# Optimization experiments

Hardware: AMD Instinct MI355X
Metric: run time of the kernel (lower is better)

## Reference

```python
import jax, jax.numpy as jnp
import numpy as np

DIM = 64
SQRT_DIM = float(np.sqrt(DIM))


def setup_inputs() -> dict:
    rng = jax.random.key(0)
    k1, k2, k3, k4 = jax.random.split(rng, 4)
    B, S, D = 16, 2048, DIM
    query = jax.random.normal(k1, (B, S, D), dtype=jnp.float32)
    key = jax.random.normal(k2, (B, S, D), dtype=jnp.float32)
    value = jax.random.normal(k3, (B, S, D), dtype=jnp.float32)
    mask = jax.random.randint(k4, (B, S), 0, 2) == 1  # True = masked (pad)
    return {"query": query, "key": key, "value": value, "mask": mask}


def reference(query, key, value, mask):
    # score: [B, S, S]
    score = jnp.einsum('bsd,btd->bst', query, key) / SQRT_DIM
    # symmetric mask: position (i, j) masked if token i OR token j is padded
    m = jnp.logical_or(mask[:, :, None], mask[:, None, :])  # [B, S, S]
    score = jnp.where(m, -jnp.inf, score)
    attn = jax.nn.softmax(score, axis=-1)
    attn = jnp.where(m, 0.0, attn)
    context = jnp.einsum('bst,btd->bsd', attn, value)
    return (context, attn)
```

## Files before the change

### kernel.cpp

```cpp
#include <hip/hip_runtime.h>
#include <hip/hip_bf16.h>

#define NBATCH 16
#define SLEN   2048
#define DIM    64
#define TQ     64
#define NTHR   256
#define NW     4
#define PANEL  128
#define NPANEL (SLEN / PANEL)
#define PROWP  136
#define PROWK  72
#define PROWV  136

typedef __attribute__((ext_vector_type(8))) short bf16x8;
typedef __attribute__((ext_vector_type(4))) float f32x4;

__device__ inline short f2bf(float f) {
    union { __hip_bfloat16 h; short s; } u;
    u.h = __float2bfloat16(f);
    return u.s;
}
__device__ inline float bf2f(unsigned short s) {
    union { unsigned u; float f; } x;
    x.u = ((unsigned)s) << 16;
    return x.f;
}
__device__ inline bf16x8 pack8(float4 a, float4 b) {
    bf16x8 r;
    r[0] = f2bf(a.x); r[1] = f2bf(a.y); r[2] = f2bf(a.z); r[3] = f2bf(a.w);
    r[4] = f2bf(b.x); r[5] = f2bf(b.y); r[6] = f2bf(b.z); r[7] = f2bf(b.w);
    return r;
}
__device__ inline bf16x8 pack8s(float4 a, float4 b, float s) {
    bf16x8 r;
    r[0] = f2bf(a.x * s); r[1] = f2bf(a.y * s); r[2] = f2bf(a.z * s); r[3] = f2bf(a.w * s);
    r[4] = f2bf(b.x * s); r[5] = f2bf(b.y * s); r[6] = f2bf(b.z * s); r[7] = f2bf(b.w * s);
    return r;
}

__global__ __launch_bounds__(256) void preconvert_kernel(
    const float* __restrict__ K, const float* __restrict__ V,
    short* __restrict__ Kws, short* __restrict__ VTws)
{
    const int b  = blockIdx.x >> 4;
    const int p  = blockIdx.x & 15;
    const int j0 = p * PANEL;
    const int tid = threadIdx.x;
    const float* Kb = K + ((size_t)b * SLEN + j0) * DIM;
    const float* Vb = V + ((size_t)b * SLEN + j0) * DIM;
    short* Kwb  = Kws  + ((size_t)b * SLEN + j0) * DIM;
    short* VTwb = VTws + (size_t)b * DIM * SLEN;

    #pragma unroll
    for (int it = 0; it < 8; it++) {
        const int idx = it * 256 + tid;
        const int row = idx >> 4, c4 = idx & 15;
        float4 kv = *(const float4*)(Kb + (size_t)row * DIM + c4 * 4);
        const int blk = (c4 >> 1) ^ (row & 7);
        *(short4*)(Kwb + (size_t)row * DIM + blk * 8 + (c4 & 1) * 4) =
            make_short4(f2bf(kv.x), f2bf(kv.y), f2bf(kv.z), f2bf(kv.w));
    }
    #pragma unroll
    for (int it = 0; it < 2; it++) {
        const int task = it * 256 + tid;
        const int k4 = task >> 4, d4 = (task & 15) * 4;
        const int kb = k4 * 4;
        const float* vp = Vb + (size_t)kb * DIM + d4;
        float4 r0 = *(const float4*)(vp);
        float4 r1 = *(const float4*)(vp + DIM);
        float4 r2 = *(const float4*)(vp + 2 * DIM);
        float4 r3 = *(const float4*)(vp + 3 * DIM);
        const int qn = kb >> 3, hw = kb & 7;
        *(short4*)(VTwb + (size_t)(d4 + 0) * SLEN + j0 + ((qn ^ ((d4 + 0) & 7)) * 8) + hw) =
            make_short4(f2bf(r0.x), f2bf(r1.x), f2bf(r2.x), f2bf(r3.x));
        *(short4*)(VTwb + (size_t)(d4 + 1) * SLEN + j0 + ((qn ^ ((d4 + 1) & 7)) * 8) + hw) =
            make_short4(f2bf(r0.y), f2bf(r1.y), f2bf(r2.y), f2bf(r3.y));
        *(short4*)(VTwb + (size_t)(d4 + 2) * SLEN + j0 + ((qn ^ ((d4 + 2) & 7)) * 8) + hw) =
            make_short4(f2bf(r0.z), f2bf(r1.z), f2bf(r2.z), f2bf(r3.z));
        *(short4*)(VTwb + (size_t)(d4 + 3) * SLEN + j0 + ((qn ^ ((d4 + 3) & 7)) * 8) + hw) =
            make_short4(f2bf(r0.w), f2bf(r1.w), f2bf(r2.w), f2bf(r3.w));
    }
}

__device__ __forceinline__ void stage_k_panel(const short* __restrict__ Kwb, int j0,
                                              short* sdst, int w, int l) {
    const short* src = Kwb + (size_t)j0 * DIM + w * 512 + l * 8;
    short* dst = sdst + w * 512;
    #pragma unroll
    for (int i = 0; i < 4; i++)
        __builtin_amdgcn_global_load_lds((const unsigned int*)(src + i * 2048),
                                         (unsigned int*)(dst + i * 2048), 16, 0, 0);
}
__device__ __forceinline__ void stage_v_panel(const short* __restrict__ VTwb, int j0,
                                              short* sdst, int w, int l) {
    #pragma unroll
    for (int i = 0; i < 4; i++) {
        const int d0 = (w * 4 + i) * 4;
        __builtin_amdgcn_global_load_lds(
            (const unsigned int*)(VTwb + (size_t)(d0 + (l >> 4)) * SLEN + j0 + (l & 15) * 8),
            (unsigned int*)(sdst + d0 * PANEL), 16, 0, 0);
    }
}

#define MFMA16(a, bb, cc) __builtin_amdgcn_mfma_f32_16x16x32_bf16((a), (bb), (cc), 0, 0, 0)

__global__ __launch_bounds__(NTHR, 3) void sdpa_kernel(
    const float* __restrict__ Q, const short* __restrict__ Kws,
    const short* __restrict__ VTws, const int* __restrict__ M,
    float* __restrict__ outCtx, float* __restrict__ outAttn)
{
    __shared__ __align__(16) short sK[PANEL * DIM];
    __shared__ __align__(16) short sVT[DIM * PANEL];
    __shared__ __align__(16) short sP[NW * 16 * PROWP];
    __shared__ short sMaskBf[SLEN];

    const int tid = threadIdx.x;
    const int w = tid >> 6, l = tid & 63, g = l >> 4, c = l & 15;
    const int wg = (blockIdx.x & 7) * (NBATCH * (SLEN / TQ) / 8) + (blockIdx.x >> 3);
    const int b  = wg >> 5;
    const int i0 = (wg & 31) * TQ;
    const int i0w = i0 + w * 16;

    const short* Kwb  = Kws  + (size_t)b * SLEN * DIM;
    const short* VTwb = VTws + (size_t)b * DIM * SLEN;
    const int*   Mb   = M + b * SLEN;

    bf16x8 qa0, qa1;
    {
        const float* qp = Q + ((size_t)b * SLEN + i0w + c) * DIM + g * 8;
        qa0 = pack8s(*(const float4*)(qp),      *(const float4*)(qp + 4),  0.125f);
        qa1 = pack8s(*(const float4*)(qp + 32), *(const float4*)(qp + 36), 0.125f);
    }

    stage_k_panel(Kwb, 0, sK, w, l);
    #pragma unroll
    for (int i = 0; i < 8; i++) {
        const int idx = i * NTHR + tid;
        sMaskBf[idx] = Mb[idx] ? (short)0 : (short)0x3F80;
    }
    __syncthreads();

    float rsum[4] = {0.f, 0.f, 0.f, 0.f};
    for (int p = 0; p < NPANEL; p++) {
        const short* cur = (p & 1) ? sVT : sK;
        if (p < NPANEL - 1)
            stage_k_panel(Kwb, (p + 1) * PANEL, (p & 1) ? sK : sVT, w, l);
        const int j0 = p * PANEL;
        #pragma unroll
        for (int jt = 0; jt < 8; jt++) {
            const short* kr = cur + (jt * 16 + c) * DIM;
            bf16x8 kb0 = *(const bf16x8*)(kr + ((g ^ (c & 7)) * 8));
            bf16x8 kb1 = *(const bf16x8*)(kr + (((g + 4) ^ (c & 7)) * 8));
            f32x4 acc = {0.f, 0.f, 0.f, 0.f};
            acc = MFMA16(qa0, kb0, acc);
            acc = MFMA16(qa1, kb1, acc);
            const float em = bf2f((unsigned short)sMaskBf[j0 + jt * 16 + c]);
            #pragma unroll
            for (int r = 0; r < 4; r++)
                rsum[r] += __expf(acc[r]) * em;
        }
        __syncthreads();
    }

    stage_k_panel(Kwb, 0, sK, w, l);
    stage_v_panel(VTwb, 0, sVT, w, l);

    #pragma unroll
    for (int off = 1; off < 16; off <<= 1) {
        #pragma unroll
        for (int r = 0; r < 4; r++)
            rsum[r] += __shfl_xor(rsum[r], off, 64);
    }
    float scv[4];
    #pragma unroll
    for (int r = 0; r < 4; r++) {
        const bool rm = sMaskBf[i0w + g * 4 + r] == 0;
        scv[r] = (rm || rsum[r] <= 0.f) ? 0.f : 1.f / rsum[r];
    }

    short* sPw = sP + w * 16 * PROWP;
    f32x4 pv[4];
    #pragma unroll
    for (int nt = 0; nt < 4; nt++) pv[nt] = (f32x4){0.f, 0.f, 0.f, 0.f};

    __syncthreads();

    for (int p = 0; p < NPANEL; p++) {
        const int j0 = p * PANEL;
        #pragma unroll
        for (int jt = 0; jt < 8; jt++) {
            const short* kr = sK + (jt * 16 + c) * DIM;
            bf16x8 kb0 = *(const bf16x8*)(kr + ((g ^ (c & 7)) * 8));
            bf16x8 kb1 = *(const bf16x8*)(kr + (((g + 4) ^ (c & 7)) * 8));
            f32x4 acc = {0.f, 0.f, 0.f, 0.f};
            acc = MFMA16(qa0, kb0, acc);
            acc = MFMA16(qa1, kb1, acc);
            const float em = bf2f((unsigned short)sMaskBf[j0 + jt * 16 + c]);
            #pragma unroll
            for (int r = 0; r < 4; r++)
                sPw[(g * 4 + r) * PROWP + jt * 16 + c] =
                    f2bf(__expf(acc[r]) * em * scv[r]);
        }
        #pragma unroll
        for (int ks = 0; ks < 4; ks++) {
            bf16x8 af = *(const bf16x8*)(sPw + c * PROWP + ks * 32 + g * 8);
            #pragma unroll
            for (int nt = 0; nt < 4; nt++) {
                const int d = nt * 16 + c;
                bf16x8 bfrag = *(const bf16x8*)(sVT + d * PANEL + (((ks * 4 + g) ^ (d & 7)) * 8));
                pv[nt] = MFMA16(af, bfrag, pv[nt]);
            }
        }
        __syncthreads();
        if (p < NPANEL - 1) {
            stage_k_panel(Kwb, j0 + PANEL, sK, w, l);
            stage_v_panel(VTwb, j0 + PANEL, sVT, w, l);
        }
        const size_t rowBase = (size_t)b * SLEN + i0w;
        #pragma unroll
        for (int it = 0; it < 8; it++) {
            const int idx = it * 64 + l;
            const int row = idx >> 5, col4 = idx & 31;
            const unsigned short* pp = (const unsigned short*)sPw + row * PROWP + col4 * 4;
            ushort4 p4 = *(const ushort4*)(pp);
            f32x4 o = {bf2f(p4.x), bf2f(p4.y), bf2f(p4.z), bf2f(p4.w)};
            __builtin_nontemporal_store(o, (f32x4*)(outAttn + (rowBase + row) * SLEN + j0 + col4 * 4));
        }
        __syncthreads();
    }

    #pragma unroll
    for (int nt = 0; nt < 4; nt++) {
        #pragma unroll
        for (int r = 0; r < 4; r++)
            __builtin_nontemporal_store(pv[nt][r],
                outCtx + ((size_t)b * SLEN + i0w + g * 4 + r) * DIM + nt * 16 + c);
    }
}

__global__ __launch_bounds__(NTHR, 3) void sdpa_kernel_fb(
    const float* __restrict__ Q, const float* __restrict__ K,
    const float* __restrict__ V, const int* __restrict__ M,
    float* __restrict__ outCtx, float* __restrict__ outAttn)
{
    __shared__ __align__(16) short sK[128 * PROWK];
    __shared__ __align__(16) short sVT[64 * PROWV];
    __shared__ __align__(16) short sP[NW * 16 * PROWP];
    __shared__ float sMask[PANEL];

    const int tid = threadIdx.x;
    const int w = tid >> 6, l = tid & 63, g = l >> 4, c = l & 15;
    const int b  = blockIdx.x >> 5;
    const int i0 = (blockIdx.x & 31) * TQ;
    const int i0w = i0 + w * 16;

    const float* Kb = K + (size_t)b * SLEN * DIM;
    const float* Vb = V + (size_t)b * SLEN * DIM;
    const int*   Mb = M + b * SLEN;

    bf16x8 qa0, qa1;
    {
        const float* qp = Q + ((size_t)b * SLEN + i0w + c) * DIM + g * 8;
        qa0 = pack8(*(const float4*)(qp),      *(const float4*)(qp + 4));
        qa1 = pack8(*(const float4*)(qp + 32), *(const float4*)(qp + 36));
    }

    const float scl = 0.125f;
    float rsum[4] = {0.f, 0.f, 0.f, 0.f};

    for (int p = 0; p < NPANEL; p++) {
        const int j0 = p * PANEL;
        #pragma unroll
        for (int it = 0; it < 8; it++) {
            const int idx = it * NTHR + tid;
            const int row = idx >> 4, c4 = idx & 15;
            float4 kv = *(const float4*)(Kb + (size_t)(j0 + row) * DIM + c4 * 4);
            *(short4*)(sK + row * PROWK + c4 * 4) =
                make_short4(f2bf(kv.x), f2bf(kv.y), f2bf(kv.z), f2bf(kv.w));
        }
        if (tid < PANEL) sMask[tid] = Mb[j0 + tid] ? 0.f : 1.f;
        __syncthreads();
        #pragma unroll
        for (int jt = 0; jt < 8; jt++) {
            const short* kr = sK + (jt * 16 + c) * PROWK + g * 8;
            bf16x8 kb0 = *(const bf16x8*)(kr);
            bf16x8 kb1 = *(const bf16x8*)(kr + 32);
            f32x4 acc = {0.f, 0.f, 0.f, 0.f};
            acc = MFMA16(qa0, kb0, acc);
            acc = MFMA16(qa1, kb1, acc);
            const float em = sMask[jt * 16 + c];
            #pragma unroll
            for (int r = 0; r < 4; r++)
                rsum[r] += __expf(acc[r] * scl) * em;
        }
        __syncthreads();
    }
    #pragma unroll
    for (int off = 1; off < 16; off <<= 1) {
        #pragma unroll
        for (int r = 0; r < 4; r++)
            rsum[r] += __shfl_xor(rsum[r], off, 64);
    }
    float scv[4];
    #pragma unroll
    for (int r = 0; r < 4; r++) {
        const int rm = Mb[i0w + g * 4 + r];
        scv[r] = (rm || rsum[r] <= 0.f) ? 0.f : 1.f / rsum[r];
    }

    short* sPw = sP + w * 16 * PROWP;
    f32x4 pv[4];
    #pragma unroll
    for (int nt = 0; nt < 4; nt++) pv[nt] = (f32x4){0.f, 0.f, 0.f, 0.f};

    for (int p = 0; p < NPANEL; p++) {
        const int j0 = p * PANEL;
        #pragma unroll
        for (int it = 0; it < 8; it++) {
            const int idx = it * NTHR + tid;
            const int row = idx >> 4, c4 = idx & 15;
            float4 kv = *(const float4*)(Kb + (size_t)(j0 + row) * DIM + c4 * 4);
            *(short4*)(sK + row * PROWK + c4 * 4) =
                make_short4(f2bf(kv.x), f2bf(kv.y), f2bf(kv.z), f2bf(kv.w));
        }
        #pragma unroll
        for (int it = 0; it < 2; it++) {
            const int task = it * NTHR + tid;
            const int k4 = task >> 4, d4g = task & 15;
            const int kb = k4 * 4, d4 = d4g * 4;
            const int colb = kb ^ ((d4g & 3) << 3);
            const float* vp = Vb + (size_t)(j0 + kb) * DIM + d4;
            float4 r0 = *(const float4*)(vp);
            float4 r1 = *(const float4*)(vp + DIM);
            float4 r2 = *(const float4*)(vp + 2 * DIM);
            float4 r3 = *(const float4*)(vp + 3 * DIM);
            *(short4*)(sVT + (d4 + 0) * PROWV + colb) =
                make_short4(f2bf(r0.x), f2bf(r1.x), f2bf(r2.x), f2bf(r3.x));
            *(short4*)(sVT + (d4 + 1) * PROWV + colb) =
                make_short4(f2bf(r0.y), f2bf(r1.y), f2bf(r2.y), f2bf(r3.y));
            *(short4*)(sVT + (d4 + 2) * PROWV + colb) =
                make_short4(f2bf(r0.z), f2bf(r1.z), f2bf(r2.z), f2bf(r3.z));
            *(short4*)(sVT + (d4 + 3) * PROWV + colb) =
                make_short4(f2bf(r0.w), f2bf(r1.w), f2bf(r2.w), f2bf(r3.w));
        }
        if (tid < PANEL) sMask[tid] = Mb[j0 + tid] ? 0.f : 1.f;
        __syncthreads();

        #pragma unroll
        for (int jt = 0; jt < 8; jt++) {
            const short* kr = sK + (jt * 16 + c) * PROWK + g * 8;
            bf16x8 kb0 = *(const bf16x8*)(kr);
            bf16x8 kb1 = *(const bf16x8*)(kr + 32);
            f32x4 acc = {0.f, 0.f, 0.f, 0.f};
            acc = MFMA16(qa0, kb0, acc);
            acc = MFMA16(qa1, kb1, acc);
            const float em = sMask[jt * 16 + c];
            #pragma unroll
            for (int r = 0; r < 4; r++)
                sPw[(g * 4 + r) * PROWP + jt * 16 + c] =
                    f2bf(__expf(acc[r] * scl) * em * scv[r]);
        }
        #pragma unroll
        for (int ks = 0; ks < 4; ks++) {
            bf16x8 af = *(const bf16x8*)(sPw + c * PROWP + ks * 32 + g * 8);
            #pragma unroll
            for (int nt = 0; nt < 4; nt++) {
                const int d = nt * 16 + c;
                const int gp = g ^ ((d >> 2) & 3);
                bf16x8 bfrag = *(const bf16x8*)(sVT + d * PROWV + ks * 32 + gp * 8);
                pv[nt] = MFMA16(af, bfrag, pv[nt]);
            }
        }
        const size_t rowBase = (size_t)b * SLEN + i0w;
        #pragma unroll
        for (int it = 0; it < 8; it++) {
            const int idx = it * 64 + l;
            const int row = idx >> 5, col4 = idx & 31;
            const unsigned short* pp = (const unsigned short*)sPw + row * PROWP + col4 * 4;
            ushort4 p4 = *(const ushort4*)(pp);
            float4 o = {bf2f(p4.x), bf2f(p4.y), bf2f(p4.z), bf2f(p4.w)};
            *(float4*)(outAttn + (rowBase + row) * SLEN + j0 + col4 * 4) = o;
        }
        __syncthreads();
    }

    #pragma unroll
    for (int nt = 0; nt < 4; nt++) {
        #pragma unroll
        for (int r = 0; r < 4; r++)
            outCtx[((size_t)b * SLEN + i0w + g * 4 + r) * DIM + nt * 16 + c] = pv[nt][r];
    }
}

extern "C" void kernel_launch(void* const* d_in, const int* in_sizes, int n_in,
                              void* d_out, int out_size, void* d_ws, size_t ws_size,
                              hipStream_t stream) {
    const float* Q = (const float*)d_in[0];
    const float* K = (const float*)d_in[1];
    const float* V = (const float*)d_in[2];
    const int*   M = (const int*)d_in[3];
    float* outCtx  = (float*)d_out;
    float* outAttn = (float*)d_out + (size_t)NBATCH * SLEN * DIM;
    dim3 grid(NBATCH * (SLEN / TQ));

    const size_t nElem = (size_t)NBATCH * SLEN * DIM;
    const size_t wsNeed = nElem * 2 * sizeof(short);
    if (d_ws != nullptr && ws_size >= wsNeed) {
        short* Kws  = (short*)d_ws;
        short* VTws = Kws + nElem;
        preconvert_kernel<<<dim3(NBATCH * NPANEL), 256, 0, stream>>>(K, V, Kws, VTws);
        sdpa_kernel<<<grid, NTHR, 0, stream>>>(Q, Kws, VTws, M, outCtx, outAttn);
    } else {
        sdpa_kernel_fb<<<grid, NTHR, 0, stream>>>(Q, K, V, M, outCtx, outAttn);
    }
}
```

Measured before the change: 318.0 us.

## Read K and V^T fragments directly from global memory instead of LDS staging

Removes the LDS double-buffered staging of K and V^T panels and the block-wide barriers around it. MFMA operand fragments now load straight from the preconverted bf16 workspaces in global memory, with the XOR swizzle dropped from the preconversion layout. This cuts LDS usage and synchronisation, which may raise occupancy. The cost is that every wave fetches the same K/V data separately through the cache hierarchy, and those loads are no longer prefetched ahead of use.

```diff
diff --git a/kernel.cpp b/kernel.cpp
--- a/kernel.cpp
+++ b/kernel.cpp
@@ -57,8 +57,7 @@
         const int idx = it * 256 + tid;
         const int row = idx >> 4, c4 = idx & 15;
         float4 kv = *(const float4*)(Kb + (size_t)row * DIM + c4 * 4);
-        const int blk = (c4 >> 1) ^ (row & 7);
-        *(short4*)(Kwb + (size_t)row * DIM + blk * 8 + (c4 & 1) * 4) =
+        *(short4*)(Kwb + (size_t)row * DIM + c4 * 4) =
             make_short4(f2bf(kv.x), f2bf(kv.y), f2bf(kv.z), f2bf(kv.w));
     }
     #pragma unroll
@@ -71,35 +70,14 @@
         float4 r1 = *(const float4*)(vp + DIM);
         float4 r2 = *(const float4*)(vp + 2 * DIM);
         float4 r3 = *(const float4*)(vp + 3 * DIM);
-        const int qn = kb >> 3, hw = kb & 7;
-        *(short4*)(VTwb + (size_t)(d4 + 0) * SLEN + j0 + ((qn ^ ((d4 + 0) & 7)) * 8) + hw) =
+        *(short4*)(VTwb + (size_t)(d4 + 0) * SLEN + j0 + kb) =
             make_short4(f2bf(r0.x), f2bf(r1.x), f2bf(r2.x), f2bf(r3.x));
-        *(short4*)(VTwb + (size_t)(d4 + 1) * SLEN + j0 + ((qn ^ ((d4 + 1) & 7)) * 8) + hw) =
+        *(short4*)(VTwb + (size_t)(d4 + 1) * SLEN + j0 + kb) =
             make_short4(f2bf(r0.y), f2bf(r1.y), f2bf(r2.y), f2bf(r3.y));
-        *(short4*)(VTwb + (size_t)(d4 + 2) * SLEN + j0 + ((qn ^ ((d4 + 2) & 7)) * 8) + hw) =
+        *(short4*)(VTwb + (size_t)(d4 + 2) * SLEN + j0 + kb) =
             make_short4(f2bf(r0.z), f2bf(r1.z), f2bf(r2.z), f2bf(r3.z));
-        *(short4*)(VTwb + (size_t)(d4 + 3) * SLEN + j0 + ((qn ^ ((d4 + 3) & 7)) * 8) + hw) =
+        *(short4*)(VTwb + (size_t)(d4 + 3) * SLEN + j0 + kb) =
             make_short4(f2bf(r0.w), f2bf(r1.w), f2bf(r2.w), f2bf(r3.w));
-    }
-}
-
-__device__ __forceinline__ void stage_k_panel(const short* __restrict__ Kwb, int j0,
-                                              short* sdst, int w, int l) {
-    const short* src = Kwb + (size_t)j0 * DIM + w * 512 + l * 8;
-    short* dst = sdst + w * 512;
-    #pragma unroll
-    for (int i = 0; i < 4; i++)
-        __builtin_amdgcn_global_load_lds((const unsigned int*)(src + i * 2048),
-                                         (unsigned int*)(dst + i * 2048), 16, 0, 0);
-}
-__device__ __forceinline__ void stage_v_panel(const short* __restrict__ VTwb, int j0,
-                                              short* sdst, int w, int l) {
-    #pragma unroll
-    for (int i = 0; i < 4; i++) {
-        const int d0 = (w * 4 + i) * 4;
-        __builtin_amdgcn_global_load_lds(
-            (const unsigned int*)(VTwb + (size_t)(d0 + (l >> 4)) * SLEN + j0 + (l & 15) * 8),
-            (unsigned int*)(sdst + d0 * PANEL), 16, 0, 0);
     }
 }
 
@@ -110,8 +88,6 @@
     const short* __restrict__ VTws, const int* __restrict__ M,
     float* __restrict__ outCtx, float* __restrict__ outAttn)
 {
-    __shared__ __align__(16) short sK[PANEL * DIM];
-    __shared__ __align__(16) short sVT[DIM * PANEL];
     __shared__ __align__(16) short sP[NW * 16 * PROWP];
     __shared__ short sMaskBf[SLEN];
 
@@ -133,7 +109,6 @@
         qa1 = pack8s(*(const float4*)(qp + 32), *(const float4*)(qp + 36), 0.125f);
     }
 
-    stage_k_panel(Kwb, 0, sK, w, l);
     #pragma unroll
     for (int i = 0; i < 8; i++) {
         const int idx = i * NTHR + tid;
@@ -143,15 +118,12 @@
 
     float rsum[4] = {0.f, 0.f, 0.f, 0.f};
     for (int p = 0; p < NPANEL; p++) {
-        const short* cur = (p & 1) ? sVT : sK;
-        if (p < NPANEL - 1)
-            stage_k_panel(Kwb, (p + 1) * PANEL, (p & 1) ? sK : sVT, w, l);
         const int j0 = p * PANEL;
         #pragma unroll
         for (int jt = 0; jt < 8; jt++) {
-            const short* kr = cur + (jt * 16 + c) * DIM;
-            bf16x8 kb0 = *(const bf16x8*)(kr + ((g ^ (c & 7)) * 8));
-            bf16x8 kb1 = *(const bf16x8*)(kr + (((g + 4) ^ (c & 7)) * 8));
+            const short* kr = Kwb + (size_t)(j0 + jt * 16 + c) * DIM + g * 8;
+            bf16x8 kb0 = *(const bf16x8*)(kr);
+            bf16x8 kb1 = *(const bf16x8*)(kr + 32);
             f32x4 acc = {0.f, 0.f, 0.f, 0.f};
             acc = MFMA16(qa0, kb0, acc);
             acc = MFMA16(qa1, kb1, acc);
@@ -160,12 +132,7 @@
             for (int r = 0; r < 4; r++)
                 rsum[r] += __expf(acc[r]) * em;
         }
-        __syncthreads();
-    }
-
-    stage_k_panel(Kwb, 0, sK, w, l);
-    stage_v_panel(VTwb, 0, sVT, w, l);
-
+    }
     #pragma unroll
     for (int off = 1; off < 16; off <<= 1) {
         #pragma unroll
@@ -184,15 +151,13 @@
     #pragma unroll
     for (int nt = 0; nt < 4; nt++) pv[nt] = (f32x4){0.f, 0.f, 0.f, 0.f};
 
-    __syncthreads();
-
     for (int p = 0; p < NPANEL; p++) {
         const int j0 = p * PANEL;
         #pragma unroll
         for (int jt = 0; jt < 8; jt++) {
-            const short* kr = sK + (jt * 16 + c) * DIM;
-            bf16x8 kb0 = *(const bf16x8*)(kr + ((g ^ (c & 7)) * 8));
-            bf16x8 kb1 = *(const bf16x8*)(kr + (((g + 4) ^ (c & 7)) * 8));
+            const short* kr = Kwb + (size_t)(j0 + jt * 16 + c) * DIM + g * 8;
+            bf16x8 kb0 = *(const bf16x8*)(kr);
+            bf16x8 kb1 = *(const bf16x8*)(kr + 32);
             f32x4 acc = {0.f, 0.f, 0.f, 0.f};
             acc = MFMA16(qa0, kb0, acc);
             acc = MFMA16(qa1, kb1, acc);
@@ -207,15 +172,10 @@
             bf16x8 af = *(const bf16x8*)(sPw + c * PROWP + ks * 32 + g * 8);
             #pragma unroll
             for (int nt = 0; nt < 4; nt++) {
-                const int d = nt * 16 + c;
-                bf16x8 bfrag = *(const bf16x8*)(sVT + d * PANEL + (((ks * 4 + g) ^ (d & 7)) * 8));
+                bf16x8 bfrag = *(const bf16x8*)(VTwb +
+                    (size_t)(nt * 16 + c) * SLEN + j0 + ks * 32 + g * 8);
                 pv[nt] = MFMA16(af, bfrag, pv[nt]);
             }
-        }
-        __syncthreads();
-        if (p < NPANEL - 1) {
-            stage_k_panel(Kwb, j0 + PANEL, sK, w, l);
-            stage_v_panel(VTwb, j0 + PANEL, sVT, w, l);
         }
         const size_t rowBase = (size_t)b * SLEN + i0w;
         #pragma unroll
@@ -227,7 +187,6 @@
             f32x4 o = {bf2f(p4.x), bf2f(p4.y), bf2f(p4.z), bf2f(p4.w)};
             __builtin_nontemporal_store(o, (f32x4*)(outAttn + (rowBase + row) * SLEN + j0 + col4 * 4));
         }
-        __syncthreads();
     }
 
     #pragma unroll
```

Result: slower. 429.7 us (+35.1%).

## Pre-pack V into MFMA fragment order and read it directly from global

Applied to the files above, without the earlier changes.

The preconvert kernel now writes V in bf16 laid out exactly as the per-lane B-operand fragments of the PV MFMA. The main kernel reads these fragments straight from global memory (L2-resident) with a two-deep register prefetch, so V is no longer staged through LDS. The freed LDS buffer double-buffers K in the second pass, which removes one __syncthreads per panel and overlaps the next K load with compute. The cost is global-memory latency on the V reads inside the MFMA loop and a redundant per-wave reload of V from cache.

```diff
diff --git a/kernel.cpp b/kernel.cpp
--- a/kernel.cpp
+++ b/kernel.cpp
@@ -41,7 +41,7 @@
 
 __global__ __launch_bounds__(256) void preconvert_kernel(
     const float* __restrict__ K, const float* __restrict__ V,
-    short* __restrict__ Kws, short* __restrict__ VTws)
+    short* __restrict__ Kws, short* __restrict__ Vp)
 {
     const int b  = blockIdx.x >> 4;
     const int p  = blockIdx.x & 15;
@@ -49,8 +49,8 @@
     const int tid = threadIdx.x;
     const float* Kb = K + ((size_t)b * SLEN + j0) * DIM;
     const float* Vb = V + ((size_t)b * SLEN + j0) * DIM;
-    short* Kwb  = Kws  + ((size_t)b * SLEN + j0) * DIM;
-    short* VTwb = VTws + (size_t)b * DIM * SLEN;
+    short* Kwb = Kws + ((size_t)b * SLEN + j0) * DIM;
+    short* Vpb = Vp  + (size_t)b * SLEN * DIM + (size_t)p * 8192;
 
     #pragma unroll
     for (int it = 0; it < 8; it++) {
@@ -64,22 +64,20 @@
     #pragma unroll
     for (int it = 0; it < 2; it++) {
         const int task = it * 256 + tid;
-        const int k4 = task >> 4, d4 = (task & 15) * 4;
-        const int kb = k4 * 4;
+        const int kb = (task >> 4) * 4, d4 = (task & 15) * 4;
         const float* vp = Vb + (size_t)kb * DIM + d4;
         float4 r0 = *(const float4*)(vp);
         float4 r1 = *(const float4*)(vp + DIM);
         float4 r2 = *(const float4*)(vp + 2 * DIM);
         float4 r3 = *(const float4*)(vp + 3 * DIM);
-        const int qn = kb >> 3, hw = kb & 7;
-        *(short4*)(VTwb + (size_t)(d4 + 0) * SLEN + j0 + ((qn ^ ((d4 + 0) & 7)) * 8) + hw) =
-            make_short4(f2bf(r0.x), f2bf(r1.x), f2bf(r2.x), f2bf(r3.x));
-        *(short4*)(VTwb + (size_t)(d4 + 1) * SLEN + j0 + ((qn ^ ((d4 + 1) & 7)) * 8) + hw) =
-            make_short4(f2bf(r0.y), f2bf(r1.y), f2bf(r2.y), f2bf(r3.y));
-        *(short4*)(VTwb + (size_t)(d4 + 2) * SLEN + j0 + ((qn ^ ((d4 + 2) & 7)) * 8) + hw) =
-            make_short4(f2bf(r0.z), f2bf(r1.z), f2bf(r2.z), f2bf(r3.z));
-        *(short4*)(VTwb + (size_t)(d4 + 3) * SLEN + j0 + ((qn ^ ((d4 + 3) & 7)) * 8) + hw) =
-            make_short4(f2bf(r0.w), f2bf(r1.w), f2bf(r2.w), f2bf(r3.w));
+        const int ks = (kb >> 5) & 3, gg = (kb >> 3) & 3, e = kb & 7;
+        #define VDST(dd) (Vpb + ((size_t)((ks * 4 + ((d4 + dd) >> 4)) * 64 \
+                              + gg * 16 + ((d4 + dd) & 15))) * 8 + e)
+        *(short4*)VDST(0) = make_short4(f2bf(r0.x), f2bf(r1.x), f2bf(r2.x), f2bf(r3.x));
+        *(short4*)VDST(1) = make_short4(f2bf(r0.y), f2bf(r1.y), f2bf(r2.y), f2bf(r3.y));
+        *(short4*)VDST(2) = make_short4(f2bf(r0.z), f2bf(r1.z), f2bf(r2.z), f2bf(r3.z));
+        *(short4*)VDST(3) = make_short4(f2bf(r0.w), f2bf(r1.w), f2bf(r2.w), f2bf(r3.w));
+        #undef VDST
     }
 }
 
@@ -92,26 +90,16 @@
         __builtin_amdgcn_global_load_lds((const unsigned int*)(src + i * 2048),
                                          (unsigned int*)(dst + i * 2048), 16, 0, 0);
 }
-__device__ __forceinline__ void stage_v_panel(const short* __restrict__ VTwb, int j0,
-                                              short* sdst, int w, int l) {
-    #pragma unroll
-    for (int i = 0; i < 4; i++) {
-        const int d0 = (w * 4 + i) * 4;
-        __builtin_amdgcn_global_load_lds(
-            (const unsigned int*)(VTwb + (size_t)(d0 + (l >> 4)) * SLEN + j0 + (l & 15) * 8),
-            (unsigned int*)(sdst + d0 * PANEL), 16, 0, 0);
-    }
-}
 
 #define MFMA16(a, bb, cc) __builtin_amdgcn_mfma_f32_16x16x32_bf16((a), (bb), (cc), 0, 0, 0)
 
 __global__ __launch_bounds__(NTHR, 3) void sdpa_kernel(
     const float* __restrict__ Q, const short* __restrict__ Kws,
-    const short* __restrict__ VTws, const int* __restrict__ M,
+    const short* __restrict__ Vp, const int* __restrict__ M,
     float* __restrict__ outCtx, float* __restrict__ outAttn)
 {
-    __shared__ __align__(16) short sK[PANEL * DIM];
-    __shared__ __align__(16) short sVT[DIM * PANEL];
+    __shared__ __align__(16) short sK0[PANEL * DIM];
+    __shared__ __align__(16) short sK1[PANEL * DIM];
     __shared__ __align__(16) short sP[NW * 16 * PROWP];
     __shared__ short sMaskBf[SLEN];
 
@@ -122,9 +110,9 @@
     const int i0 = (wg & 31) * TQ;
     const int i0w = i0 + w * 16;
 
-    const short* Kwb  = Kws  + (size_t)b * SLEN * DIM;
-    const short* VTwb = VTws + (size_t)b * DIM * SLEN;
-    const int*   Mb   = M + b * SLEN;
+    const short* Kwb = Kws + (size_t)b * SLEN * DIM;
+    const short* Vwb = Vp  + (size_t)b * SLEN * DIM;
+    const int*   Mb  = M + b * SLEN;
 
     bf16x8 qa0, qa1;
     {
@@ -133,7 +121,7 @@
         qa1 = pack8s(*(const float4*)(qp + 32), *(const float4*)(qp + 36), 0.125f);
     }
 
-    stage_k_panel(Kwb, 0, sK, w, l);
+    stage_k_panel(Kwb, 0, sK0, w, l);
     #pragma unroll
     for (int i = 0; i < 8; i++) {
         const int idx = i * NTHR + tid;
@@ -143,9 +131,9 @@
 
     float rsum[4] = {0.f, 0.f, 0.f, 0.f};
     for (int p = 0; p < NPANEL; p++) {
-        const short* cur = (p & 1) ? sVT : sK;
+        const short* cur = (p & 1) ? sK1 : sK0;
         if (p < NPANEL - 1)
-            stage_k_panel(Kwb, (p + 1) * PANEL, (p & 1) ? sK : sVT, w, l);
+            stage_k_panel(Kwb, (p + 1) * PANEL, (p & 1) ? sK0 : sK1, w, l);
         const int j0 = p * PANEL;
         #pragma unroll
         for (int jt = 0; jt < 8; jt++) {
@@ -163,8 +151,7 @@
         __syncthreads();
     }
 
-    stage_k_panel(Kwb, 0, sK, w, l);
-    stage_v_panel(VTwb, 0, sVT, w, l);
+    stage_k_panel(Kwb, 0, sK0, w, l);
 
     #pragma unroll
     for (int off = 1; off < 16; off <<= 1) {
@@ -188,9 +175,13 @@
 
     for (int p = 0; p < NPANEL; p++) {
         const int j0 = p * PANEL;
+        if (p < NPANEL - 1)
+            stage_k_panel(Kwb, j0 + PANEL, (p & 1) ? sK0 : sK1, w, l);
+        const short* kbuf = (p & 1) ? sK1 : sK0;
+
         #pragma unroll
         for (int jt = 0; jt < 8; jt++) {
-            const short* kr = sK + (jt * 16 + c) * DIM;
+            const short* kr = kbuf + (jt * 16 + c) * DIM;
             bf16x8 kb0 = *(const bf16x8*)(kr + ((g ^ (c & 7)) * 8));
             bf16x8 kb1 = *(const bf16x8*)(kr + (((g + 4) ^ (c & 7)) * 8));
             f32x4 acc = {0.f, 0.f, 0.f, 0.f};
@@ -202,20 +193,20 @@
                 sPw[(g * 4 + r) * PROWP + jt * 16 + c] =
                     f2bf(__expf(acc[r]) * em * scv[r]);
         }
-        #pragma unroll
-        for (int ks = 0; ks < 4; ks++) {
-            bf16x8 af = *(const bf16x8*)(sPw + c * PROWP + ks * 32 + g * 8);
-            #pragma unroll
-            for (int nt = 0; nt < 4; nt++) {
-                const int d = nt * 16 + c;
-                bf16x8 bfrag = *(const bf16x8*)(sVT + d * PANEL + (((ks * 4 + g) ^ (d & 7)) * 8));
-                pv[nt] = MFMA16(af, bfrag, pv[nt]);
+        {
+            const short* vb = Vwb + (size_t)p * 8192 + l * 8;
+            bf16x8 v0 = *(const bf16x8*)(vb);
+            bf16x8 v1 = *(const bf16x8*)(vb + 512);
+            bf16x8 af;
+            #pragma unroll
+            for (int i = 0; i < 16; i++) {
+                bf16x8 cur = v0;
+                v0 = v1;
+                if (i + 2 < 16) v1 = *(const bf16x8*)(vb + (i + 2) * 512);
+                if ((i & 3) == 0)
+                    af = *(const bf16x8*)(sPw + c * PROWP + (i >> 2) * 32 + g * 8);
+                pv[i & 3] = MFMA16(af, cur, pv[i & 3]);
             }
-        }
-        __syncthreads();
-        if (p < NPANEL - 1) {
-            stage_k_panel(Kwb, j0 + PANEL, sK, w, l);
-            stage_v_panel(VTwb, j0 + PANEL, sVT, w, l);
         }
         const size_t rowBase = (size_t)b * SLEN + i0w;
         #pragma unroll
@@ -225,7 +216,8 @@
             const unsigned short* pp = (const unsigned short*)sPw + row * PROWP + col4 * 4;
             ushort4 p4 = *(const ushort4*)(pp);
             f32x4 o = {bf2f(p4.x), bf2f(p4.y), bf2f(p4.z), bf2f(p4.w)};
-            __builtin_nontemporal_store(o, (f32x4*)(outAttn + (rowBase + row) * SLEN + j0 + col4 * 4));
+            __builtin_nontemporal_store(o,
+                (f32x4*)(outAttn + (rowBase + row) * SLEN + j0 + col4 * 4));
         }
         __syncthreads();
     }
@@ -407,10 +399,10 @@
     const size_t nElem = (size_t)NBATCH * SLEN * DIM;
     const size_t wsNeed = nElem * 2 * sizeof(short);
     if (d_ws != nullptr && ws_size >= wsNeed) {
-        short* Kws  = (short*)d_ws;
-        short* VTws = Kws + nElem;
-        preconvert_kernel<<<dim3(NBATCH * NPANEL), 256, 0, stream>>>(K, V, Kws, VTws);
-        sdpa_kernel<<<grid, NTHR, 0, stream>>>(Q, Kws, VTws, M, outCtx, outAttn);
+        short* Kws = (short*)d_ws;
+        short* Vpp = Kws + nElem;
+        preconvert_kernel<<<dim3(NBATCH * NPANEL), 256, 0, stream>>>(K, V, Kws, Vpp);
+        sdpa_kernel<<<grid, NTHR, 0, stream>>>(Q, Kws, Vpp, M, outCtx, outAttn);
     } else {
         sdpa_kernel_fb<<<grid, NTHR, 0, stream>>>(Q, K, V, M, outCtx, outAttn);
     }
```

New measurement: 311.2 us. -2.1%, faster.
